# Optimization experiments

Hardware: AMD Instinct MI355X
Metric: run time of the kernel (lower is better)

## Reference

```python
import jax, jax.numpy as jnp
import numpy as np
import math

B, S, DM, H, DH = 2, 2048, 1024, 16, 64  # batch, seq, d_model, heads, head_dim


def setup_inputs() -> dict:
    key = jax.random.key(0)
    ks = jax.random.split(key, 4)
    scale = 0.02
    return {
        "hidden_states": jax.random.normal(ks[0], (B, S, DM), jnp.float32),
        "Wq": jax.random.normal(ks[1], (DM, DM), jnp.float32) * scale,
        "bq": jnp.zeros((DM,), jnp.float32),
        "Wk": jax.random.normal(ks[2], (DM, DM), jnp.float32) * scale,
        "bk": jnp.zeros((DM,), jnp.float32),
        "Wv": jax.random.normal(ks[3], (DM, DM), jnp.float32) * scale,
        "bv": jnp.zeros((DM,), jnp.float32),
    }


def reference(hidden_states, Wq, bq, Wk, bk, Wv, bv):
    b, s, _ = hidden_states.shape

    def proj(W, bias):
        # torch Linear: x @ W.T + b, then transpose_for_scores -> [B,H,S,Dh]
        x = hidden_states @ W.T + bias
        return x.reshape(b, s, H, DH).transpose(0, 2, 1, 3)

    query = proj(Wq, bq)
    key = proj(Wk, bk)
    value = proj(Wv, bv)

    # qk_matmul input calibration stats (abs-max over whole tensor)
    q_max = jax.lax.stop_gradient(jnp.max(jnp.abs(query)))
    kT_max = jax.lax.stop_gradient(jnp.max(jnp.abs(key)))  # transpose doesn't change abs-max

    attn_weights = jnp.einsum('bhqd,bhkd->bhqk', query, key)  # [B,H,S,S]
    qk_out_max = jax.lax.stop_gradient(jnp.max(jnp.abs(attn_weights)))

    attn_weights = attn_weights / math.sqrt(DH)
    attn_weights = jax.nn.softmax(attn_weights.astype(jnp.float32), axis=-1).astype(query.dtype)
    # eval mode: dropout p=0.0; head_mask is None

    # v_matmul input stats; note source also records attn_weights abs-max as 'v_matmul_out' (faithful)
    aw_max = jax.lax.stop_gradient(jnp.max(jnp.abs(attn_weights)))
    v_max = jax.lax.stop_gradient(jnp.max(jnp.abs(value)))
    v_out_max = aw_max  # source bug: re-reads attn_weights for v_matmul_out

    attn_output = jnp.einsum('bhqk,bhkd->bhqd', attn_weights, value)
    attn_output = attn_output.transpose(0, 2, 1, 3).reshape(b, s, H * DH)
    return attn_output, q_max, kT_max, qk_out_max, aw_max, v_max, v_out_max
```

## Files before the change

### kernel.cpp

```cpp
#include <hip/hip_runtime.h>
#include <hip/hip_bf16.h>
#include <stdint.h>

typedef __attribute__((ext_vector_type(8))) short short8;
typedef __attribute__((ext_vector_type(4))) short short4v;
typedef __attribute__((ext_vector_type(4))) float f32x4;

#define MFMA(a, b, c) __builtin_amdgcn_mfma_f32_16x16x32_bf16((a), (b), (c), 0, 0, 0)

#define C1 0.18033688011112042f
#define INV_C1 5.545177444479562f

static __device__ __forceinline__ unsigned int f2bf2(float x, float y) {
  union { __hip_bfloat162 h; unsigned int u; } c;
  c.h = __float22bfloat162_rn(make_float2(x, y));
  return c.u;
}

static __device__ __forceinline__ float exp2_fast(float x) {
  float r;
  asm("v_exp_f32 %0, %1" : "=v"(r) : "v"(x));
  return r;
}
static __device__ __forceinline__ unsigned int cvtpk(float lo, float hi) {
  unsigned int r;
  asm("v_cvt_pk_bf16_f32 %0, %1, %2" : "=v"(r) : "v"(lo), "v"(hi));
  return r;
}

static __device__ __forceinline__ void atomic_max_f32(float* addr, float v) {
  atomicMax((int*)addr, __float_as_int(v));
}

static __device__ __forceinline__ void gl_lds16(const void* g, void* l) {
  __builtin_amdgcn_global_load_lds(
      (const __attribute__((address_space(1))) void*)g,
      (__attribute__((address_space(3))) void*)l, 16, 0, 0);
}

__global__ __launch_bounds__(256) void k_cvt(
    const float* __restrict__ X, const float* __restrict__ Wq,
    const float* __restrict__ Wk, const float* __restrict__ Wv,
    short* __restrict__ Xb, short* __restrict__ Wb) {
  const int y = blockIdx.y;
  const float* src;
  short* dst;
  int n;
  if (y == 0) {
    src = X; dst = Xb; n = 4096 * 1024;
  } else {
    src = (y == 1) ? Wq : (y == 2) ? Wk : Wv;
    dst = Wb + (y - 1) * 1048576;
    n = 1048576;
  }
  const int i = (blockIdx.x * 256 + threadIdx.x) * 8;
  if (i >= n) return;
  const float4 a = *(const float4*)(src + i);
  const float4 b = *(const float4*)(src + i + 4);
  union { unsigned int u[4]; short8 s; } P;
  P.u[0] = f2bf2(a.x, a.y);
  P.u[1] = f2bf2(a.z, a.w);
  P.u[2] = f2bf2(b.x, b.y);
  P.u[3] = f2bf2(b.z, b.w);
  *(short8*)(dst + i) = P.s;
}

__global__ __launch_bounds__(256) void k_qkv(
    const short* __restrict__ Xb, const short* __restrict__ Wball,
    const float* __restrict__ bq, const float* __restrict__ bk,
    const float* __restrict__ bv,
    short* __restrict__ Qo, short* __restrict__ Ko, short* __restrict__ Vo,
    float* __restrict__ stats) {
  const int fid = (blockIdx.z * 32 + blockIdx.y) * 8 + blockIdx.x;
  const int sid = (fid & 7) * 96 + (fid >> 3);
  const int colb = sid & 7;
  const int zy = sid >> 3;
  const int z = zy >> 5;
  const int yb = zy & 31;

  const short* W = Wball + z * 1048576;
  const float* bias = (z == 0) ? bq : (z == 1) ? bk : bv;
  short* out = (z == 0) ? Qo : (z == 1) ? Ko : Vo;
  const bool qk = (z < 2);

  __shared__ __align__(16) short B0s[8192];
  __shared__ __align__(16) short B1s[8192];
  __shared__ __align__(16) short B2s[8192];
  __shared__ float red[4];

  const int t = threadIdx.x;
  const int lane = t & 63;
  const int w = t >> 6;
  const int l16 = lane & 15, quad = lane >> 4;
  const int wr = (w >> 1) * 64, wc = (w & 1) * 64;
  const int row0 = yb * 128;
  const int col0 = colb * 128;

  const short* ag = Xb + (size_t)(row0 + (w & 1) * 64 + lane) * 1024 + (w >> 1) * 8;
  const short* bg = W + (size_t)(col0 + (w & 1) * 64 + lane) * 1024 + (w >> 1) * 8;

  const int f0b = qk ? 4096 : 0, f0r = qk ? wc : wr;
  const int f1b = qk ? 0 : 4096, f1r = qk ? wr : wc;
  const int cq = quad * 1024;

  f32x4 acc[4][4];
#pragma unroll
  for (int i = 0; i < 4; ++i)
#pragma unroll
    for (int j = 0; j < 4; ++j) acc[i][j] = {0.f, 0.f, 0.f, 0.f};

#define STAGE(buf, ks_)                                      \
  do {                                                       \
    gl_lds16(ag + (ks_), (buf) + w * 512);                   \
    gl_lds16(ag + (ks_) + 16, (buf) + (4 + w) * 512);        \
    gl_lds16(bg + (ks_), (buf) + 4096 + w * 512);            \
    gl_lds16(bg + (ks_) + 16, (buf) + 4096 + (4 + w) * 512); \
  } while (0)

#define COMPUTE(buf)                                                   \
  do {                                                                 \
    short8 fr0[4], fr1[4];                                             \
    _Pragma("unroll") for (int a = 0; a < 4; ++a)                      \
        fr0[a] = *(const short8*)&(buf)[f0b + cq + (f0r + a * 16 + l16) * 8]; \
    _Pragma("unroll") for (int b = 0; b < 4; ++b)                      \
        fr1[b] = *(const short8*)&(buf)[f1b + cq + (f1r + b * 16 + l16) * 8]; \
    _Pragma("unroll") for (int a = 0; a < 4; ++a)                      \
        _Pragma("unroll") for (int b = 0; b < 4; ++b)                  \
            acc[a][b] = MFMA(fr0[a], fr1[b], acc[a][b]);               \
  } while (0)

#define WAITBAR(n)                                                          \
  do {                                                                      \
    asm volatile("s_waitcnt lgkmcnt(0) vmcnt(" #n ")\n\ts_barrier" ::: "memory"); \
    __builtin_amdgcn_sched_barrier(0);                                      \
  } while (0)

  STAGE(B0s, 0);
  STAGE(B1s, 32);
  WAITBAR(4);
  int ks = 64;
#pragma unroll
  for (int i = 0; i < 10; ++i) {
    STAGE(B2s, ks); ks += 32; COMPUTE(B0s); WAITBAR(4);
    STAGE(B0s, ks); ks += 32; COMPUTE(B1s); WAITBAR(4);
    STAGE(B1s, ks); ks += 32; COMPUTE(B2s); WAITBAR(4);
  }
  COMPUTE(B0s);
  WAITBAR(0);
  COMPUTE(B1s);
#undef STAGE
#undef COMPUTE
#undef WAITBAR

  const float qs = (z == 0) ? C1 : 1.0f;
  float amax = 0.f;
  if (qk) {
#pragma unroll
    for (int a = 0; a < 4; ++a) {
      const int dg = col0 + wc + a * 16 + quad * 4;
      const float4 b4 = *(const float4*)&bias[dg];
      const int h = dg >> 6, dl = dg & 63;
#pragma unroll
      for (int b = 0; b < 4; ++b) {
        const int sg = row0 + wr + b * 16 + l16;
        const float y0 = acc[a][b][0] + b4.x;
        const float y1 = acc[a][b][1] + b4.y;
        const float y2 = acc[a][b][2] + b4.z;
        const float y3 = acc[a][b][3] + b4.w;
        amax = fmaxf(amax, fmaxf(fmaxf(fabsf(y0), fabsf(y1)), fmaxf(fabsf(y2), fabsf(y3))));
        union { unsigned int u[2]; short4v s; } pk;
        pk.u[0] = cvtpk(y0 * qs, y1 * qs);
        pk.u[1] = cvtpk(y2 * qs, y3 * qs);
        const int bidx = sg >> 11, sl = sg & 2047;
        *(short4v*)&out[(size_t)(((bidx << 4) | h) * 2048 + sl) * 64 + dl] = pk.s;
      }
    }
  } else {
#pragma unroll
    for (int a = 0; a < 4; ++a) {
      const int sg = row0 + wr + a * 16 + quad * 4;
      const int bidx = sg >> 11, sl = sg & 2047;
#pragma unroll
      for (int b = 0; b < 4; ++b) {
        const int dg = col0 + wc + b * 16 + l16;
        const float bvf = bias[dg];
        const int h = dg >> 6, dl = dg & 63;
        const float y0 = acc[a][b][0] + bvf;
        const float y1 = acc[a][b][1] + bvf;
        const float y2 = acc[a][b][2] + bvf;
        const float y3 = acc[a][b][3] + bvf;
        amax = fmaxf(amax, fmaxf(fmaxf(fabsf(y0), fabsf(y1)), fmaxf(fabsf(y2), fabsf(y3))));
        union { unsigned int u[2]; short4v s; } pk;
        pk.u[0] = cvtpk(y0, y1);
        pk.u[1] = cvtpk(y2, y3);
        *(short4v*)&out[(size_t)(((bidx << 4) | h) * 64 + dl) * 2048 + sl] = pk.s;
      }
    }
  }
#pragma unroll
  for (int off = 32; off > 0; off >>= 1)
    amax = fmaxf(amax, __shfl_xor(amax, off, 64));
  if (lane == 0) red[w] = amax;
  __syncthreads();
  if (t == 0) {
    float m = fmaxf(fmaxf(red[0], red[1]), fmaxf(red[2], red[3]));
    atomic_max_f32(&stats[z], m);
  }
}

__global__ __launch_bounds__(512) void k_attn(
    const short* __restrict__ Q, const short* __restrict__ K,
    const short* __restrict__ V, float* __restrict__ O,
    float* __restrict__ stats) {
  const int fid = blockIdx.y * 16 + blockIdx.x;
  const int sid = ((fid & 7) << 6) + (fid >> 3);
  const int bh = sid >> 4;
  const int q0 = (sid & 15) << 7;
  const short* Qh = Q + (size_t)bh * 2048 * 64;
  const short* Kh = K + (size_t)bh * 2048 * 64;
  const short* Vh = V + (size_t)bh * 2048 * 64;

  __shared__ __align__(16) short Ks[64 * 64];
  __shared__ __align__(16) short Vts[64 * 64];
  __shared__ __align__(16) short Ps[8][16 * 64];
  __shared__ float redA[8], redB[8];

  const int t = threadIdx.x, lane = t & 63, w = t >> 6;
  const int l16 = lane & 15, quad = lane >> 4;
  const int srow = t >> 3;
  const int sslot = t & 7;
  const int wslot = (sslot ^ (srow & 7)) * 8;
  const int rsw = (l16 & 7);
  short* myPs = &Ps[w][0];

  short8 bq0, bq1;
  {
    const short* qsrc = Qh + (q0 + w * 16 + l16) * 64 + quad * 8;
    bq0 = *(const short8*)qsrc;
    bq1 = *(const short8*)(qsrc + 32);
  }

  float m_lane = -1e30f, l_lane = 0.f, xmin_lane = 1e30f;
  f32x4 o_acc[4];
#pragma unroll
  for (int jn = 0; jn < 4; ++jn) o_acc[jn] = {0.f, 0.f, 0.f, 0.f};
  const f32x4 zero = {0.f, 0.f, 0.f, 0.f};

  const int ksl0 = (quad ^ rsw) * 8;
  const int ksl1 = ((quad ^ rsw) ^ 4) * 8;

  short8 pk0 = *(const short8*)(Kh + srow * 64 + sslot * 8);
  short8 pv0 = *(const short8*)(Vh + srow * 2048 + sslot * 8);

  for (int kt = 0; kt < 32; ++kt) {
    __syncthreads();
    *(short8*)&Ks[srow * 64 + wslot] = pk0;
    *(short8*)&Vts[srow * 64 + wslot] = pv0;
    {
      const int ktn = (kt < 31) ? kt + 1 : 31;
      pk0 = *(const short8*)(Kh + (ktn * 64 + srow) * 64 + sslot * 8);
      pv0 = *(const short8*)(Vh + srow * 2048 + ktn * 64 + sslot * 8);
    }
    __syncthreads();

    f32x4 sacc[4];
#pragma unroll
    for (int j = 0; j < 4; ++j) {
      const int kb = (j * 16 + l16) * 64;
      short8 kf0 = *(const short8*)&Ks[kb + ksl0];
      short8 kf1 = *(const short8*)&Ks[kb + ksl1];
      sacc[j] = MFMA(kf1, bq1, MFMA(kf0, bq0, zero));
    }

    {
      float pmax = m_lane, psum = l_lane, xmn = xmin_lane;
#pragma unroll
      for (int j = 0; j < 4; ++j) {
        const float x0 = sacc[j][0], x1 = sacc[j][1];
        const float x2 = sacc[j][2], x3 = sacc[j][3];
        pmax = fmaxf(fmaxf(x0, fmaxf(x1, x2)), fmaxf(x3, pmax));
        xmn = fminf(fminf(x0, fminf(x1, x2)), fminf(x3, xmn));
        const float e0 = exp2_fast(x0), e1 = exp2_fast(x1);
        const float e2 = exp2_fast(x2), e3 = exp2_fast(x3);
        psum += (e0 + e1) + (e2 + e3);
        union { unsigned int u[2]; short4v s; } pk;
        pk.u[0] = cvtpk(e0, e1);
        pk.u[1] = cvtpk(e2, e3);
        *(short4v*)&myPs[l16 * 64 + ((j * 16 + quad * 4) ^ (rsw << 3))] = pk.s;
      }
      m_lane = pmax;
      l_lane = psum;
      xmin_lane = xmn;
    }
    asm volatile("" ::: "memory");

#pragma unroll
    for (int tstep = 0; tstep < 2; ++tstep) {
      const int psl = (tstep * 32 + quad * 8) ^ (rsw << 3);
      short8 ap = *(const short8*)&myPs[l16 * 64 + psl];
#pragma unroll
      for (int jn = 0; jn < 4; ++jn) {
        short8 vf = *(const short8*)&Vts[(jn * 16 + l16) * 64 + psl];
        o_acc[jn] = MFMA(ap, vf, o_acc[jn]);
      }
    }
    asm volatile("" ::: "memory");
  }

  float l = l_lane;
  l += __shfl_xor(l, 16, 64);
  l += __shfl_xor(l, 32, 64);
  float m = m_lane;
  m = fmaxf(m, __shfl_xor(m, 16, 64));
  m = fmaxf(m, __shfl_xor(m, 32, 64));
  float xm = xmin_lane;
  xm = fminf(xm, __shfl_xor(xm, 16, 64));
  xm = fminf(xm, __shfl_xor(xm, 32, 64));
  float aw = exp2_fast(m) / l;
  float qkx = fmaxf(m, -xm);

  const int bidx = bh >> 4, h = bh & 15;
  float linv[4];
#pragma unroll
  for (int r = 0; r < 4; ++r)
    linv[r] = 1.0f / __shfl(l, quad * 4 + r, 16);
#pragma unroll
  for (int jn = 0; jn < 4; ++jn) {
    const int d = jn * 16 + l16;
#pragma unroll
    for (int r = 0; r < 4; ++r) {
      const int s_row = q0 + w * 16 + quad * 4 + r;
      O[((size_t)(bidx * 2048 + s_row) * 1024) + h * 64 + d] =
          o_acc[jn][r] * linv[r];
    }
  }

#pragma unroll
  for (int off = 32; off > 0; off >>= 1) {
    qkx = fmaxf(qkx, __shfl_xor(qkx, off, 64));
    aw = fmaxf(aw, __shfl_xor(aw, off, 64));
  }
  if (lane == 0) {
    redA[w] = qkx;
    redB[w] = aw;
  }
  __syncthreads();
  if (t == 0) {
    float a = redA[0], b = redB[0];
#pragma unroll
    for (int i = 1; i < 8; ++i) {
      a = fmaxf(a, redA[i]);
      b = fmaxf(b, redB[i]);
    }
    atomic_max_f32(&stats[3], a * INV_C1);
    atomic_max_f32(&stats[4], b);
  }
}

__global__ void k_fin(const float* __restrict__ stats, float* __restrict__ out) {
  const int i = threadIdx.x;
  if (i == 0) out[0] = stats[0];
  if (i == 1) out[1] = stats[1];
  if (i == 2) out[2] = stats[3];
  if (i == 3) out[3] = stats[4];
  if (i == 4) out[4] = stats[2];
  if (i == 5) out[5] = stats[4];
}

extern "C" void kernel_launch(void* const* d_in, const int* in_sizes, int n_in,
                              void* d_out, int out_size, void* d_ws, size_t ws_size,
                              hipStream_t stream) {
  const float* X = (const float*)d_in[0];
  const float* Wq = (const float*)d_in[1];
  const float* bq = (const float*)d_in[2];
  const float* Wk = (const float*)d_in[3];
  const float* bk = (const float*)d_in[4];
  const float* Wv = (const float*)d_in[5];
  const float* bv = (const float*)d_in[6];
  float* out = (float*)d_out;

  float* stats = (float*)d_ws;
  short* base = (short*)((char*)d_ws + 4096);
  short* Qb = base;
  short* Kb = base + 4194304;
  short* Vb = base + 8388608;
  short* Xb = base + 12582912;
  short* Wb = base + 16777216;

  k_cvt<<<dim3(2048, 4), 256, 0, stream>>>(X, Wq, Wk, Wv, Xb, Wb);
  k_qkv<<<dim3(8, 32, 3), 256, 0, stream>>>(Xb, Wb, bq, bk, bv, Qb, Kb, Vb, stats);
  k_attn<<<dim3(16, 32), 512, 0, stream>>>(Qb, Kb, Vb, out, stats);
  k_fin<<<1, 64, 0, stream>>>(stats, out + 4194304);
}
```

Measured before the change: 194.8 us.

## Pre-tile bf16 X and W in conversion kernel for contiguous LDS staging loads

The fp32-to-bf16 conversion kernel now writes X and the weights in a blocked layout: 128-row tiles, with each 32-column k-slab split into 8-element chunks laid out row-contiguously. The QKV GEMM staging loads then read fully contiguous 1KB spans per wave instead of strided 16-byte pieces from 64 different rows. This is meant to improve global-load coalescing in the direct-to-LDS copies. In exchange the conversion kernel's stores become scattered, and the index math must exactly match what the GEMM expects.

```diff
diff --git a/kernel.cpp b/kernel.cpp
--- a/kernel.cpp
+++ b/kernel.cpp
@@ -43,18 +43,18 @@
     const float* __restrict__ Wk, const float* __restrict__ Wv,
     short* __restrict__ Xb, short* __restrict__ Wb) {
   const int y = blockIdx.y;
+  const int i = (blockIdx.x * 256 + threadIdx.x) * 8;
   const float* src;
-  short* dst;
-  int n;
+  short* dstbase;
   if (y == 0) {
-    src = X; dst = Xb; n = 4096 * 1024;
+    if (i >= 4096 * 1024) return;
+    src = X;
+    dstbase = Xb;
   } else {
+    if (i >= 1048576) return;
     src = (y == 1) ? Wq : (y == 2) ? Wk : Wv;
-    dst = Wb + (y - 1) * 1048576;
-    n = 1048576;
-  }
-  const int i = (blockIdx.x * 256 + threadIdx.x) * 8;
-  if (i >= n) return;
+    dstbase = Wb + (y - 1) * 1048576;
+  }
   const float4 a = *(const float4*)(src + i);
   const float4 b = *(const float4*)(src + i + 4);
   union { unsigned int u[4]; short8 s; } P;
@@ -62,7 +62,10 @@
   P.u[1] = f2bf2(a.z, a.w);
   P.u[2] = f2bf2(b.x, b.y);
   P.u[3] = f2bf2(b.z, b.w);
-  *(short8*)(dst + i) = P.s;
+  const int s = i >> 10, c0 = i & 1023;
+  const int off = (((s >> 7) * 32 + (c0 >> 5)) * 4 + ((c0 >> 3) & 3)) * 1024 +
+                  (s & 127) * 8;
+  *(short8*)(dstbase + off) = P.s;
 }
 
 __global__ __launch_bounds__(256) void k_qkv(
@@ -78,7 +81,6 @@
   const int z = zy >> 5;
   const int yb = zy & 31;
 
-  const short* W = Wball + z * 1048576;
   const float* bias = (z == 0) ? bq : (z == 1) ? bk : bv;
   short* out = (z == 0) ? Qo : (z == 1) ? Ko : Vo;
   const bool qk = (z < 2);
@@ -96,8 +98,8 @@
   const int row0 = yb * 128;
   const int col0 = colb * 128;
 
-  const short* ag = Xb + (size_t)(row0 + (w & 1) * 64 + lane) * 1024 + (w >> 1) * 8;
-  const short* bg = W + (size_t)(col0 + (w & 1) * 64 + lane) * 1024 + (w >> 1) * 8;
+  const short* ag = Xb + yb * 131072 + w * 512 + lane * 8;
+  const short* bg = Wball + z * 1048576 + colb * 131072 + w * 512 + lane * 8;
 
   const int f0b = qk ? 4096 : 0, f0r = qk ? wc : wr;
   const int f1b = qk ? 0 : 4096, f1r = qk ? wr : wc;
@@ -109,12 +111,12 @@
 #pragma unroll
     for (int j = 0; j < 4; ++j) acc[i][j] = {0.f, 0.f, 0.f, 0.f};
 
-#define STAGE(buf, ks_)                                      \
-  do {                                                       \
-    gl_lds16(ag + (ks_), (buf) + w * 512);                   \
-    gl_lds16(ag + (ks_) + 16, (buf) + (4 + w) * 512);        \
-    gl_lds16(bg + (ks_), (buf) + 4096 + w * 512);            \
-    gl_lds16(bg + (ks_) + 16, (buf) + 4096 + (4 + w) * 512); \
+#define STAGE(buf, ko_)                                  \
+  do {                                                   \
+    gl_lds16(ag + (ko_), (buf) + w * 512);               \
+    gl_lds16(ag + (ko_) + 2048, (buf) + 2048 + w * 512); \
+    gl_lds16(bg + (ko_), (buf) + 4096 + w * 512);        \
+    gl_lds16(bg + (ko_) + 2048, (buf) + 6144 + w * 512); \
   } while (0)
 
 #define COMPUTE(buf)                                                   \
@@ -136,14 +138,14 @@
   } while (0)
 
   STAGE(B0s, 0);
-  STAGE(B1s, 32);
+  STAGE(B1s, 4096);
   WAITBAR(4);
-  int ks = 64;
+  int ks = 8192;
 #pragma unroll
   for (int i = 0; i < 10; ++i) {
-    STAGE(B2s, ks); ks += 32; COMPUTE(B0s); WAITBAR(4);
-    STAGE(B0s, ks); ks += 32; COMPUTE(B1s); WAITBAR(4);
-    STAGE(B1s, ks); ks += 32; COMPUTE(B2s); WAITBAR(4);
+    STAGE(B2s, ks); ks += 4096; COMPUTE(B0s); WAITBAR(4);
+    STAGE(B0s, ks); ks += 4096; COMPUTE(B1s); WAITBAR(4);
+    STAGE(B1s, ks); ks += 4096; COMPUTE(B2s); WAITBAR(4);
   }
   COMPUTE(B0s);
   WAITBAR(0);
```

After: 181.1 us. -7.0%, faster.
